# Kernel optimization log

Hardware: AMD Instinct MI355X
Metric: run time of the kernel (lower is better)

The kernel has to match this reference:

```python
import jax, jax.numpy as jnp
import numpy as np

EPS = 1e-5
N_HEAD = 16


def layernorm(x, g, b):
    mu = jnp.mean(x, axis=-1, keepdims=True)
    var = jnp.mean(jnp.square(x - mu), axis=-1, keepdims=True)
    return (x - mu) * jax.lax.rsqrt(var + EPS) * g + b


def setup_inputs() -> dict:
    key = jax.random.key(0)
    ks = jax.random.split(key, 8)
    B, S, D = 4, 2048, 1024
    F = 4 * D
    s = 0.02
    return {
        "h": jax.random.normal(ks[0], (B, S, D), jnp.float32),
        "ln1_g": jnp.ones((D,), jnp.float32),
        "ln1_b": jnp.zeros((D,), jnp.float32),
        "wq": jax.random.normal(ks[1], (D, D), jnp.float32) * s,
        "bq": jnp.zeros((D,), jnp.float32),
        "wk": jax.random.normal(ks[2], (D, D), jnp.float32) * s,
        "bk": jnp.zeros((D,), jnp.float32),
        "wv": jax.random.normal(ks[3], (D, D), jnp.float32) * s,
        "bv": jnp.zeros((D,), jnp.float32),
        "wo": jax.random.normal(ks[4], (D, D), jnp.float32) * s,
        "bo": jnp.zeros((D,), jnp.float32),
        "ln2_g": jnp.ones((D,), jnp.float32),
        "ln2_b": jnp.zeros((D,), jnp.float32),
        "wfc": jax.random.normal(ks[5], (F, D), jnp.float32) * s,
        "bfc": jnp.zeros((F,), jnp.float32),
        "wproj": jax.random.normal(ks[6], (D, F), jnp.float32) * s,
        "bproj": jnp.zeros((D,), jnp.float32),
    }


def reference(h, ln1_g, ln1_b, wq, bq, wk, bk, wv, bv, wo, bo,
              ln2_g, ln2_b, wfc, bfc, wproj, bproj):
    B, S, D = h.shape
    H = N_HEAD
    Dh = D // H

    # --- attention sub-block ---
    r = h
    x = layernorm(h, ln1_g, ln1_b)
    q = (x @ wq.T + bq).reshape(B, S, H, Dh)
    k = (x @ wk.T + bk).reshape(B, S, H, Dh)
    v = (x @ wv.T + bv).reshape(B, S, H, Dh)

    scores = jnp.einsum("bqhd,bkhd->bhqk", q, k) / jnp.sqrt(jnp.float32(Dh))
    causal = jnp.tril(jnp.ones((S, S), bool))  # [S,S]
    scores = jnp.where(causal, scores, jnp.finfo(scores.dtype).min)
    probs = jax.nn.softmax(scores, axis=-1)
    o = jnp.einsum("bhqk,bkhd->bqhd", probs, v).reshape(B, S, D)
    h = r + (o @ wo.T + bo)

    # --- MLP sub-block ---
    r = h
    x = layernorm(h, ln2_g, ln2_b)
    x = jax.nn.gelu(x @ wfc.T + bfc, approximate=True)  # NewGELU (tanh)
    h = r + (x @ wproj.T + bproj)
    return h
```

## Files before the change

kernel.cpp:

```cpp
#include <hip/hip_runtime.h>
#include <hip/hip_bf16.h>
#include <stdint.h>


typedef short bf16x8 __attribute__((ext_vector_type(8)));
typedef float f32x4  __attribute__((ext_vector_type(4)));
typedef float f32x16 __attribute__((ext_vector_type(16)));
typedef short s16x4  __attribute__((ext_vector_type(4)));

__device__ __forceinline__ short f2bf(float f) {
  union { float f; uint32_t u; } a;
  a.f = f;
  uint32_t r = a.u + 0x7fffu + ((a.u >> 16) & 1u);
  return (short)(r >> 16);
}

__device__ __forceinline__ unsigned cvt_pk_bf16(float lo, float hi_) {
  unsigned r;
  asm("v_cvt_pk_bf16_f32 %0, %1, %2" : "=v"(r) : "v"(lo), "v"(hi_));
  return r;
}

__device__ __forceinline__ float ex2(float x) {
  float r;
  asm("v_exp_f32 %0, %1" : "=v"(r) : "v"(x));
  return r;
}

__device__ __forceinline__ float rcp(float x) {
  float r;
  asm("v_rcp_f32 %0, %1" : "=v"(r) : "v"(x));
  return r;
}

__device__ __forceinline__ float m3(float a, float b, float c) {
  return fmaxf(fmaxf(a, b), c);
}

__device__ __forceinline__ void gload_lds16(const void* g, void* l) {
  __builtin_amdgcn_global_load_lds(
      (const __attribute__((address_space(1))) void*)g,
      (__attribute__((address_space(3))) void*)l, 16, 0, 0);
}

__device__ __forceinline__ float gelu_f(float x) {
  float y = 0.7978845608028654f * (x + 0.044715f * x * x * x);
  y = fminf(fmaxf(y, -20.f), 20.f);
  float e = __expf(2.f * y);
  return 0.5f * x * (1.f + (e - 1.f) / (e + 1.f));
}

struct W6 {
  const float* s[6];
  short* d[6];
  int off[7];
};

__global__ __launch_bounds__(256)
void cvt_all(W6 a) {
  const int i = blockIdx.x * 256 + threadIdx.x;
#pragma unroll
  for (int k = 0; k < 6; ++k) {
    if (i >= a.off[k] && i < a.off[k + 1]) {
      const int j = i - a.off[k];
      float4 v = ((const float4*)a.s[k])[j];
      s16x4 o;
      o[0] = f2bf(v.x); o[1] = f2bf(v.y); o[2] = f2bf(v.z); o[3] = f2bf(v.w);
      ((s16x4*)a.d[k])[j] = o;
    }
  }
}

__global__ __launch_bounds__(256)
void ln_fwd(const float* __restrict__ x, const float* __restrict__ g,
            const float* __restrict__ b, short* __restrict__ y) {
  const long row = blockIdx.x;
  const int t = threadIdx.x;
  const float4 xv = ((const float4*)(x + row * 1024))[t];
  float s  = xv.x + xv.y + xv.z + xv.w;
  float ss = xv.x * xv.x + xv.y * xv.y + xv.z * xv.z + xv.w * xv.w;
#pragma unroll
  for (int m = 1; m < 64; m <<= 1) {
    s  += __shfl_xor(s, m);
    ss += __shfl_xor(ss, m);
  }
  __shared__ float rs[4], rss[4];
  const int wid = t >> 6, lane = t & 63;
  if (lane == 0) { rs[wid] = s; rss[wid] = ss; }
  __syncthreads();
  s  = rs[0] + rs[1] + rs[2] + rs[3];
  ss = rss[0] + rss[1] + rss[2] + rss[3];
  const float mu   = s * (1.f / 1024.f);
  const float var  = ss * (1.f / 1024.f) - mu * mu;
  const float rstd = rsqrtf(var + 1e-5f);
  const float4 gv = ((const float4*)g)[t];
  const float4 bv = ((const float4*)b)[t];
  s16x4 ov;
  ov[0] = f2bf((xv.x - mu) * rstd * gv.x + bv.x);
  ov[1] = f2bf((xv.y - mu) * rstd * gv.y + bv.y);
  ov[2] = f2bf((xv.z - mu) * rstd * gv.z + bv.z);
  ov[3] = f2bf((xv.w - mu) * rstd * gv.w + bv.w);
  *(s16x4*)(y + row * 1024 + t * 4) = ov;
}

template <int OUT_BF16, int HAS_RES, int HAS_GELU, int SCALE_Q>
__global__ __launch_bounds__(256, 2)
void gemm_bt5(const short* __restrict__ A, const short* __restrict__ W,
              const float* __restrict__ bias, const float* __restrict__ res,
              void* __restrict__ out, int M, int N, int K) {
  __shared__ short As[128 * 64];
  __shared__ short Bs[256 * 64];
  const int tid = threadIdx.x;
  const int wid = tid >> 6, lane = tid & 63;
  const int l16 = lane & 15, lg = lane >> 4;
  const int wm = wid >> 1, wn = wid & 1;

  const int nbx = N >> 8;
  const int nwg = nbx * (M >> 7);
  int flat = (int)blockIdx.x;
  if ((nwg & 7) == 0) flat = (flat & 7) * (nwg >> 3) + (flat >> 3);
  const int brow = (flat / nbx) * 128, bcol = (flat % nbx) * 256;

  f32x4 acc[4][8] = {};

  const int r0 = tid >> 3, g0 = tid & 7;

  int ra[4], rb[8];
#pragma unroll
  for (int m = 0; m < 4; ++m) ra[m] = wm * 64 + m * 16 + l16;
#pragma unroll
  for (int n = 0; n < 8; ++n) rb[n] = wn * 128 + n * 16 + l16;

  for (int kt = 0; kt < K; kt += 64) {
    __syncthreads();
#pragma unroll
    for (int i = 0; i < 4; ++i) {
      const int row = i * 32 + r0;
      gload_lds16(A + (long)(brow + row) * K + kt + 8 * (g0 ^ (row & 7)),
                  &As[(i * 256 + tid) * 8]);
    }
#pragma unroll
    for (int i = 0; i < 8; ++i) {
      const int row = i * 32 + r0;
      gload_lds16(W + (long)(bcol + row) * K + kt + 8 * (g0 ^ (row & 7)),
                  &Bs[(i * 256 + tid) * 8]);
    }
    __syncthreads();

#pragma unroll
    for (int kk = 0; kk < 2; ++kk) {
      bf16x8 af[4], bf[8];
#pragma unroll
      for (int m = 0; m < 4; ++m)
        af[m] = *(const bf16x8*)&As[ra[m] * 64 + 8 * ((kk * 4 + lg) ^ (ra[m] & 7))];
#pragma unroll
      for (int n = 0; n < 8; ++n)
        bf[n] = *(const bf16x8*)&Bs[rb[n] * 64 + 8 * ((kk * 4 + lg) ^ (rb[n] & 7))];
#pragma unroll
      for (int m = 0; m < 4; ++m)
#pragma unroll
        for (int n = 0; n < 8; ++n)
          acc[m][n] = __builtin_amdgcn_mfma_f32_16x16x32_bf16(af[m], bf[n], acc[m][n], 0, 0, 0);
    }
  }

#pragma unroll
  for (int n = 0; n < 8; ++n) {
    const int col = bcol + wn * 128 + n * 16 + l16;
    const float bb = bias[col];
    const bool doScale = SCALE_Q && (col < N / 3);
#pragma unroll
    for (int m = 0; m < 4; ++m) {
#pragma unroll
      for (int j = 0; j < 4; ++j) {
        const long row = brow + wm * 64 + m * 16 + lg * 4 + j;
        float vv = acc[m][n][j] + bb;
        if (HAS_GELU) vv = gelu_f(vv);
        if (HAS_RES) vv += res[row * N + col];
        if (SCALE_Q && doScale) vv *= 0.18033688f;
        if (OUT_BF16) ((short*)out)[row * N + col] = f2bf(vv);
        else          ((float*)out)[row * N + col] = vv;
      }
    }
  }
}

template <int OUT_BF16, int HAS_RES, int HAS_GELU>
__global__ __launch_bounds__(256, 2)
void gemm_bt6(const short* __restrict__ A, const short* __restrict__ W,
              const float* __restrict__ bias, const float* __restrict__ res,
              void* __restrict__ out, int M, int N, int K) {
  __shared__ short As[128 * 64];
  __shared__ short Bs[128 * 64];
  const int tid = threadIdx.x;
  const int wid = tid >> 6, lane = tid & 63;
  const int l16 = lane & 15, lg = lane >> 4;
  const int wm = wid >> 1, wn = wid & 1;

  const int nbx = N >> 7;
  const int nwg = nbx * (M >> 7);
  int flat = (int)blockIdx.x;
  if ((nwg & 7) == 0) flat = (flat & 7) * (nwg >> 3) + (flat >> 3);
  const int brow = (flat / nbx) * 128, bcol = (flat % nbx) * 128;

  f32x4 acc[4][4] = {};

  const int r0 = tid >> 3, g0 = tid & 7;

  int ra[4], rb[4];
#pragma unroll
  for (int m = 0; m < 4; ++m) ra[m] = wm * 64 + m * 16 + l16;
#pragma unroll
  for (int n = 0; n < 4; ++n) rb[n] = wn * 64 + n * 16 + l16;

  for (int kt = 0; kt < K; kt += 64) {
    __syncthreads();
#pragma unroll
    for (int i = 0; i < 4; ++i) {
      const int row = i * 32 + r0;
      gload_lds16(A + (long)(brow + row) * K + kt + 8 * (g0 ^ (row & 7)),
                  &As[(i * 256 + tid) * 8]);
      gload_lds16(W + (long)(bcol + row) * K + kt + 8 * (g0 ^ (row & 7)),
                  &Bs[(i * 256 + tid) * 8]);
    }
    __syncthreads();

#pragma unroll
    for (int kk = 0; kk < 2; ++kk) {
      bf16x8 af[4], bf[4];
#pragma unroll
      for (int m = 0; m < 4; ++m)
        af[m] = *(const bf16x8*)&As[ra[m] * 64 + 8 * ((kk * 4 + lg) ^ (ra[m] & 7))];
#pragma unroll
      for (int n = 0; n < 4; ++n)
        bf[n] = *(const bf16x8*)&Bs[rb[n] * 64 + 8 * ((kk * 4 + lg) ^ (rb[n] & 7))];
#pragma unroll
      for (int m = 0; m < 4; ++m)
#pragma unroll
        for (int n = 0; n < 4; ++n)
          acc[m][n] = __builtin_amdgcn_mfma_f32_16x16x32_bf16(af[m], bf[n], acc[m][n], 0, 0, 0);
    }
  }

#pragma unroll
  for (int n = 0; n < 4; ++n) {
    const int col = bcol + wn * 64 + n * 16 + l16;
    const float bb = bias[col];
#pragma unroll
    for (int m = 0; m < 4; ++m) {
#pragma unroll
      for (int j = 0; j < 4; ++j) {
        const long row = brow + wm * 64 + m * 16 + lg * 4 + j;
        float vv = acc[m][n][j] + bb;
        if (HAS_GELU) vv = gelu_f(vv);
        if (HAS_RES) vv += res[row * N + col];
        if (OUT_BF16) ((short*)out)[row * N + col] = f2bf(vv);
        else          ((float*)out)[row * N + col] = vv;
      }
    }
  }
}

__global__ __launch_bounds__(256)
void transpose_v(const short* __restrict__ v, short* __restrict__ vtg,
                 int S, int ldv, int H) {
  __shared__ short t[64][66];
  const int bh = blockIdx.y, b = bh / H, hh = bh % H;
  const int s0 = blockIdx.x * 64;
  const int tid = threadIdx.x;
#pragma unroll
  for (int i = 0; i < 2; ++i) {
    const int c = i * 256 + tid;
    const int sl = c >> 3, d8 = (c & 7) * 8;
    bf16x8 vv = *(const bf16x8*)&v[((long)b * S + s0 + sl) * ldv + hh * 64 + d8];
#pragma unroll
    for (int j = 0; j < 8; ++j) t[d8 + j][sl] = vv[j];
  }
  __syncthreads();
#pragma unroll
  for (int i = 0; i < 2; ++i) {
    const int c = i * 256 + tid;
    const int dl = c >> 3, s8 = (c & 7) * 8;
    bf16x8 ov;
#pragma unroll
    for (int j = 0; j < 8; ++j) ov[j] = t[dl][s8 + j];
    *(bf16x8*)&vtg[((long)bh * 64 + dl) * S + s0 + s8] = ov;
  }
}

__global__ __launch_bounds__(256, 4)
void attn_fwd2(const short* __restrict__ qg, const short* __restrict__ kg,
               const short* __restrict__ vtg, short* __restrict__ og,
               int S, int ldq, int D, int H) {
  const int tid = threadIdx.x, wid = tid >> 6, lane = tid & 63;
  const int l31 = lane & 31, hi = lane >> 5;
  const int fid = blockIdx.x;
  const int bh = fid & 63;
  const int b = bh / H, hh = bh % H;
  static const int perm[16] = {15, 0, 8, 7, 1, 14, 6, 9, 13, 2, 10, 5, 3, 12, 4, 11};
  const int qt = perm[(fid >> 6) & 15];
  const int q0 = qt * 128;
  const long qbase = (long)b * S * ldq + hh * 64;
  const long obase = (long)b * S * D + hh * 64;
  const long vbase = (long)bh * 64 * S;

  __shared__ short Ks[2][64 * 64];
  __shared__ short Vs[2][64 * 64];

  auto STAGE = [&](int buf, int k0) {
#pragma unroll
    for (int i = 0; i < 2; ++i) {
      const int c = i * 256 + tid;
      const int row = c >> 3, gl = c & 7;
      gload_lds16(&kg[qbase + (long)(k0 + row) * ldq + 8 * (gl ^ (row & 7))],
                  &Ks[buf][(i * 256 + wid * 64) * 8]);
      gload_lds16(&vtg[vbase + (long)row * S + k0 + 8 * (gl ^ (row & 7))],
                  &Vs[buf][(i * 256 + wid * 64) * 8]);
    }
  };

  const int qw = q0 + wid * 32;
  const int qv = qw + l31;

  bf16x8 qf[4];
#pragma unroll
  for (int s = 0; s < 4; ++s)
    qf[s] = *(const bf16x8*)&qg[qbase + (long)qv * ldq + 16 * s + 8 * hi];

  f32x16 oa[2] = {};
  float mr = -3000.f, lr = 0.f;

  const int ntiles = qt * 2 + 2;

  STAGE(0, 0);
  for (int t = 0; t < ntiles; ++t) {
    const int cur = t & 1;
    const int k0 = t * 64;
    if (t + 1 < ntiles) {
      STAGE(cur ^ 1, k0 + 64);
      asm volatile("s_waitcnt vmcnt(4)" ::: "memory");
    } else {
      asm volatile("s_waitcnt vmcnt(0)" ::: "memory");
    }
    __builtin_amdgcn_s_barrier();

    if (k0 < qw + 32) {
      f32x16 st[2] = {};
#pragma unroll
      for (int s = 0; s < 4; ++s) {
        const int g = ((s << 1) | hi) ^ (l31 & 7);
        bf16x8 kf0 = *(const bf16x8*)&Ks[cur][l31 * 64 + 8 * g];
        bf16x8 kf1 = *(const bf16x8*)&Ks[cur][(32 + l31) * 64 + 8 * g];
        st[0] = __builtin_amdgcn_mfma_f32_32x32x16_bf16(kf0, qf[s], st[0], 0, 0, 0);
        st[1] = __builtin_amdgcn_mfma_f32_32x32x16_bf16(kf1, qf[s], st[1], 0, 0, 0);
      }

      const bool need_mask = (k0 + 63 > qw);
      float pv[2][16];
#pragma unroll
      for (int kb = 0; kb < 2; ++kb)
#pragma unroll
        for (int r = 0; r < 16; ++r) {
          float v = st[kb][r];
          if (need_mask) {
            const int key = k0 + kb * 32 + (r & 3) + 8 * (r >> 2) + 4 * hi;
            if (key > qv) v = -1e30f;
          }
          pv[kb][r] = v;
        }

      float rm = fmaxf(pv[0][0], pv[0][1]);
#pragma unroll
      for (int r = 2; r < 16; r += 2) rm = m3(rm, pv[0][r], pv[0][r + 1]);
#pragma unroll
      for (int r = 0; r < 16; r += 2) rm = m3(rm, pv[1][r], pv[1][r + 1]);
      rm = fmaxf(rm, __shfl_xor(rm, 32));

      const bool defer = (bool)__all(rm <= mr + 8.f);
      const float mn = defer ? mr : fmaxf(mr, rm);

      float a0 = 0.f, a1 = 0.f, a2 = 0.f, a3 = 0.f;
#pragma unroll
      for (int r = 0; r < 8; ++r) {
        float p0 = ex2(pv[0][r] - mn);      pv[0][r] = p0;      a0 += p0;
        float p1 = ex2(pv[0][8 + r] - mn);  pv[0][8 + r] = p1;  a1 += p1;
        float p2 = ex2(pv[1][r] - mn);      pv[1][r] = p2;      a2 += p2;
        float p3 = ex2(pv[1][8 + r] - mn);  pv[1][8 + r] = p3;  a3 += p3;
      }
      float ls = (a0 + a1) + (a2 + a3);
      ls += __shfl_xor(ls, 32);

      if (!defer) {
        const float alpha = ex2(mr - mn);
        lr = lr * alpha + ls;
        mr = mn;
#pragma unroll
        for (int r = 0; r < 16; ++r) {
          const int crow = (r & 3) + 8 * (r >> 2) + 4 * hi;
          const float ar = __shfl(alpha, crow | (lane & 32));
          oa[0][r] *= ar;
          oa[1][r] *= ar;
        }
      } else {
        lr += ls;
      }

      bf16x8 pa[4];
#pragma unroll
      for (int kb = 0; kb < 2; ++kb) {
        unsigned pk[8], ex[8];
#pragma unroll
        for (int i2 = 0; i2 < 8; ++i2)
          pk[i2] = cvt_pk_bf16(pv[kb][2 * i2], pv[kb][2 * i2 + 1]);
#pragma unroll
        for (int i2 = 0; i2 < 8; ++i2)
          ex[i2] = (unsigned)__shfl_xor((int)pk[i2], 32);
        union { unsigned u[4]; bf16x8 v8; } f0, f1;
        f0.u[0] = hi ? ex[2] : pk[0];
        f0.u[1] = hi ? ex[3] : pk[1];
        f0.u[2] = hi ? pk[2] : ex[0];
        f0.u[3] = hi ? pk[3] : ex[1];
        f1.u[0] = hi ? ex[6] : pk[4];
        f1.u[1] = hi ? ex[7] : pk[5];
        f1.u[2] = hi ? pk[6] : ex[4];
        f1.u[3] = hi ? pk[7] : ex[5];
        pa[2 * kb]     = f0.v8;
        pa[2 * kb + 1] = f1.v8;
      }

#pragma unroll
      for (int s = 0; s < 4; ++s) {
        const int g = ((s << 1) | hi) ^ (l31 & 7);
        bf16x8 vf0 = *(const bf16x8*)&Vs[cur][l31 * 64 + 8 * g];
        bf16x8 vf1 = *(const bf16x8*)&Vs[cur][(32 + l31) * 64 + 8 * g];
        oa[0] = __builtin_amdgcn_mfma_f32_32x32x16_bf16(pa[s], vf0, oa[0], 0, 0, 0);
        oa[1] = __builtin_amdgcn_mfma_f32_32x32x16_bf16(pa[s], vf1, oa[1], 0, 0, 0);
      }
    }

    asm volatile("s_waitcnt lgkmcnt(0)" ::: "memory");
    __builtin_amdgcn_s_barrier();
  }

  const float linv = rcp(lr);
#pragma unroll
  for (int r = 0; r < 16; ++r) {
    const int crow = (r & 3) + 8 * (r >> 2) + 4 * hi;
    const float li = __shfl(linv, crow | (lane & 32));
    const long row = qw + crow;
    og[obase + row * D + l31]      = f2bf(oa[0][r] * li);
    og[obase + row * D + 32 + l31] = f2bf(oa[1][r] * li);
  }
}

extern "C" void kernel_launch(void* const* d_in, const int* in_sizes, int n_in,
                              void* d_out, int out_size, void* d_ws, size_t ws_size,
                              hipStream_t stream) {
  (void)in_sizes; (void)n_in; (void)out_size; (void)ws_size;
  const float* h     = (const float*)d_in[0];
  const float* ln1_g = (const float*)d_in[1];
  const float* ln1_b = (const float*)d_in[2];
  const float* wq    = (const float*)d_in[3];
  const float* bq    = (const float*)d_in[4];
  const float* wk    = (const float*)d_in[5];
  const float* bk    = (const float*)d_in[6];
  const float* wv    = (const float*)d_in[7];
  const float* bv    = (const float*)d_in[8];
  const float* wo    = (const float*)d_in[9];
  const float* bo    = (const float*)d_in[10];
  const float* ln2_g = (const float*)d_in[11];
  const float* ln2_b = (const float*)d_in[12];
  const float* wfc   = (const float*)d_in[13];
  const float* bfc   = (const float*)d_in[14];
  const float* wproj = (const float*)d_in[15];
  const float* bproj = (const float*)d_in[16];

  const int B = 4, S = 2048, D = 1024, H = 16, F = 4096, T = B * S;
  const int D3 = 3 * D;

  char* ws = (char*)d_ws;
  size_t off = 0;
  auto alloc = [&](size_t bytes) {
    void* p = ws + off;
    off += (bytes + 255) & ~(size_t)255;
    return p;
  };
  short* xb   = (short*)alloc((size_t)T * D * 2);
  short* qkv  = (short*)alloc((size_t)T * D3 * 2);
  short* ob   = (short*)alloc((size_t)T * D * 2);
  float* h2   = (float*)alloc((size_t)T * D * 4);
  short* wqkvb  = (short*)alloc((size_t)D3 * D * 2);
  short* wob    = (short*)alloc((size_t)D * D * 2);
  short* wfcb   = (short*)alloc((size_t)F * D * 2);
  short* wprojb = (short*)alloc((size_t)D * F * 2);
  float* bqkv   = (float*)alloc((size_t)D3 * 4);
  short* ub  = qkv;
  short* vtg = (short*)h2;

  W6 wargs;
  const int nqq = D * D / 4;
  wargs.s[0] = wq;    wargs.d[0] = wqkvb;
  wargs.s[1] = wk;    wargs.d[1] = wqkvb + (size_t)D * D;
  wargs.s[2] = wv;    wargs.d[2] = wqkvb + (size_t)2 * D * D;
  wargs.s[3] = wo;    wargs.d[3] = wob;
  wargs.s[4] = wfc;   wargs.d[4] = wfcb;
  wargs.s[5] = wproj; wargs.d[5] = wprojb;
  wargs.off[0] = 0;
  wargs.off[1] = nqq;
  wargs.off[2] = 2 * nqq;
  wargs.off[3] = 3 * nqq;
  wargs.off[4] = 4 * nqq;
  wargs.off[5] = 4 * nqq + F * D / 4;
  wargs.off[6] = 4 * nqq + 2 * (F * D / 4);
  cvt_all<<<dim3(wargs.off[6] / 256), 256, 0, stream>>>(wargs);
  hipMemcpyAsync(bqkv,         bq, D * 4, hipMemcpyDeviceToDevice, stream);
  hipMemcpyAsync(bqkv + D,     bk, D * 4, hipMemcpyDeviceToDevice, stream);
  hipMemcpyAsync(bqkv + 2 * D, bv, D * 4, hipMemcpyDeviceToDevice, stream);

  ln_fwd<<<dim3(T), 256, 0, stream>>>(h, ln1_g, ln1_b, xb);
  gemm_bt5<1, 0, 0, 1><<<dim3((T / 128) * (D3 / 256)), 256, 0, stream>>>(
      xb, wqkvb, bqkv, nullptr, qkv, T, D3, D);
  transpose_v<<<dim3(S / 64, B * H), 256, 0, stream>>>(qkv + 2 * D, vtg, S, D3, H);
  attn_fwd2<<<dim3((S / 128) * (B * H / 64) * 64), 256, 0, stream>>>(
      qkv, qkv + D, vtg, ob, S, D3, D, H);
  gemm_bt6<0, 1, 0><<<dim3((T / 128) * (D / 128)), 256, 0, stream>>>(
      ob, wob, bo, h, h2, T, D, D);

  ln_fwd<<<dim3(T), 256, 0, stream>>>(h2, ln2_g, ln2_b, xb);
  gemm_bt5<1, 0, 1, 0><<<dim3((T / 128) * (F / 256)), 256, 0, stream>>>(
      xb, wfcb, bfc, nullptr, ub, T, F, D);
  gemm_bt6<0, 1, 0><<<dim3((T / 128) * (D / 128)), 256, 0, stream>>>(
      ub, wprojb, bproj, h2, (float*)d_out, T, D, F);
}
```

Baseline: 372.8 us.

## Replace QKV/FC GEMM with 256x256 double-buffered 8-wave pipelined kernel

Replaces the 128x256-tile, 4-wave GEMM used for the QKV and FC projections with a 256x256-tile, 512-thread kernel. It double-buffers A and B tiles in LDS and interleaves the global-to-LDS prefetch of the next K tiles with MFMA phases, using explicit barriers, waitcnts and setprio. The aim is to hide load latency and raise arithmetic intensity per tile. It uses 128KB of LDS per block, which limits occupancy, and produces fewer blocks: 384 for the QKV GEMM and 512 for FC. That risks poor wave balance across CUs.

Result: slower. 392.2 us (+5.2%).

```diff
diff --git a/kernel.cpp b/kernel.cpp
--- a/kernel.cpp
+++ b/kernel.cpp
@@ -104,82 +104,157 @@
 }
 
 template <int OUT_BF16, int HAS_RES, int HAS_GELU, int SCALE_Q>
-__global__ __launch_bounds__(256, 2)
-void gemm_bt5(const short* __restrict__ A, const short* __restrict__ W,
+__global__ __launch_bounds__(512, 2)
+void gemm256b(const short* __restrict__ A, const short* __restrict__ W,
               const float* __restrict__ bias, const float* __restrict__ res,
               void* __restrict__ out, int M, int N, int K) {
-  __shared__ short As[128 * 64];
-  __shared__ short Bs[256 * 64];
+  __shared__ short As[2][256 * 64];
+  __shared__ short Bs[2][256 * 64];
   const int tid = threadIdx.x;
   const int wid = tid >> 6, lane = tid & 63;
   const int l16 = lane & 15, lg = lane >> 4;
-  const int wm = wid >> 1, wn = wid & 1;
+  const int wm = wid >> 2, wn = wid & 3;
 
   const int nbx = N >> 8;
-  const int nwg = nbx * (M >> 7);
+  const int nwg = nbx * (M >> 8);
   int flat = (int)blockIdx.x;
   if ((nwg & 7) == 0) flat = (flat & 7) * (nwg >> 3) + (flat >> 3);
-  const int brow = (flat / nbx) * 128, bcol = (flat % nbx) * 256;
-
-  f32x4 acc[4][8] = {};
+  const int brow = (flat / nbx) * 256, bcol = (flat % nbx) * 256;
+
+  f32x4 acc[2][4][4] = {};
 
   const int r0 = tid >> 3, g0 = tid & 7;
 
-  int ra[4], rb[8];
-#pragma unroll
-  for (int m = 0; m < 4; ++m) ra[m] = wm * 64 + m * 16 + l16;
-#pragma unroll
-  for (int n = 0; n < 8; ++n) rb[n] = wn * 128 + n * 16 + l16;
-
-  for (int kt = 0; kt < K; kt += 64) {
-    __syncthreads();
-#pragma unroll
-    for (int i = 0; i < 4; ++i) {
-      const int row = i * 32 + r0;
+  auto STAGE_A = [&](int buf, int half, int kt) {
+#pragma unroll
+    for (int i = 0; i < 2; ++i) {
+      const int row = half * 128 + i * 64 + r0;
       gload_lds16(A + (long)(brow + row) * K + kt + 8 * (g0 ^ (row & 7)),
-                  &As[(i * 256 + tid) * 8]);
-    }
-#pragma unroll
-    for (int i = 0; i < 8; ++i) {
-      const int row = i * 32 + r0;
+                  &As[buf][(half * 1024 + i * 512 + tid) * 8]);
+    }
+  };
+  auto STAGE_B = [&](int buf, int half, int kt) {
+#pragma unroll
+    for (int i = 0; i < 2; ++i) {
+      const int row = half * 128 + i * 64 + r0;
       gload_lds16(W + (long)(bcol + row) * K + kt + 8 * (g0 ^ (row & 7)),
-                  &Bs[(i * 256 + tid) * 8]);
-    }
-    __syncthreads();
-
-#pragma unroll
-    for (int kk = 0; kk < 2; ++kk) {
-      bf16x8 af[4], bf[8];
-#pragma unroll
-      for (int m = 0; m < 4; ++m)
-        af[m] = *(const bf16x8*)&As[ra[m] * 64 + 8 * ((kk * 4 + lg) ^ (ra[m] & 7))];
-#pragma unroll
-      for (int n = 0; n < 8; ++n)
-        bf[n] = *(const bf16x8*)&Bs[rb[n] * 64 + 8 * ((kk * 4 + lg) ^ (rb[n] & 7))];
-#pragma unroll
-      for (int m = 0; m < 4; ++m)
-#pragma unroll
-        for (int n = 0; n < 8; ++n)
-          acc[m][n] = __builtin_amdgcn_mfma_f32_16x16x32_bf16(af[m], bf[n], acc[m][n], 0, 0, 0);
-    }
-  }
-
-#pragma unroll
-  for (int n = 0; n < 8; ++n) {
-    const int col = bcol + wn * 128 + n * 16 + l16;
+                  &Bs[buf][(half * 1024 + i * 512 + tid) * 8]);
+    }
+  };
+
+  int ra0[4], ra1[4], rb[4];
+#pragma unroll
+  for (int m = 0; m < 4; ++m) {
+    ra0[m] = wm * 128 + m * 16 + l16;
+    ra1[m] = ra0[m] + 64;
+  }
+#pragma unroll
+  for (int n = 0; n < 4; ++n) rb[n] = wn * 64 + n * 16 + l16;
+
+  const int NT = K >> 6;
+  STAGE_A(0, 0, 0); STAGE_A(0, 1, 0); STAGE_B(0, 0, 0); STAGE_B(0, 1, 0);
+  STAGE_B(1, 0, 64); STAGE_B(1, 1, 64);
+  asm volatile("s_waitcnt vmcnt(4)" ::: "memory");
+  __builtin_amdgcn_s_barrier();
+
+  for (int t = 0; t < NT; ++t) {
+    const int c = t & 1;
+    const bool s1 = (t + 1 < NT), s2 = (t + 2 < NT);
+    const int kt1 = (t + 1) << 6, kt2 = (t + 2) << 6;
+
+    bf16x8 a[4], b[4];
+
+#pragma unroll
+    for (int n = 0; n < 4; ++n)
+      b[n] = *(const bf16x8*)&Bs[c][rb[n] * 64 + 8 * (lg ^ (rb[n] & 7))];
+#pragma unroll
+    for (int m = 0; m < 4; ++m)
+      a[m] = *(const bf16x8*)&As[c][ra0[m] * 64 + 8 * (lg ^ (ra0[m] & 7))];
+    if (s1) STAGE_A(c ^ 1, 0, kt1);
+    __builtin_amdgcn_s_barrier();
+    asm volatile("s_waitcnt lgkmcnt(0)" ::: "memory");
+    __builtin_amdgcn_sched_barrier(0);
+    __builtin_amdgcn_s_setprio(1);
+#pragma unroll
+    for (int m = 0; m < 4; ++m)
+#pragma unroll
+      for (int n = 0; n < 4; ++n)
+        acc[0][m][n] = __builtin_amdgcn_mfma_f32_16x16x32_bf16(a[m], b[n], acc[0][m][n], 0, 0, 0);
+    __builtin_amdgcn_s_setprio(0);
+    __builtin_amdgcn_s_barrier();
+
+#pragma unroll
+    for (int m = 0; m < 4; ++m)
+      a[m] = *(const bf16x8*)&As[c][ra1[m] * 64 + 8 * (lg ^ (ra1[m] & 7))];
+    if (s1) STAGE_A(c ^ 1, 1, kt1);
+    __builtin_amdgcn_s_barrier();
+    asm volatile("s_waitcnt lgkmcnt(0)" ::: "memory");
+    __builtin_amdgcn_sched_barrier(0);
+    __builtin_amdgcn_s_setprio(1);
+#pragma unroll
+    for (int m = 0; m < 4; ++m)
+#pragma unroll
+      for (int n = 0; n < 4; ++n)
+        acc[1][m][n] = __builtin_amdgcn_mfma_f32_16x16x32_bf16(a[m], b[n], acc[1][m][n], 0, 0, 0);
+    __builtin_amdgcn_s_setprio(0);
+    __builtin_amdgcn_s_barrier();
+
+#pragma unroll
+    for (int n = 0; n < 4; ++n)
+      b[n] = *(const bf16x8*)&Bs[c][rb[n] * 64 + 8 * ((4 + lg) ^ (rb[n] & 7))];
+#pragma unroll
+    for (int m = 0; m < 4; ++m)
+      a[m] = *(const bf16x8*)&As[c][ra0[m] * 64 + 8 * ((4 + lg) ^ (ra0[m] & 7))];
+    __builtin_amdgcn_s_barrier();
+    asm volatile("s_waitcnt lgkmcnt(0)" ::: "memory");
+    __builtin_amdgcn_sched_barrier(0);
+    __builtin_amdgcn_s_setprio(1);
+#pragma unroll
+    for (int m = 0; m < 4; ++m)
+#pragma unroll
+      for (int n = 0; n < 4; ++n)
+        acc[0][m][n] = __builtin_amdgcn_mfma_f32_16x16x32_bf16(a[m], b[n], acc[0][m][n], 0, 0, 0);
+    __builtin_amdgcn_s_setprio(0);
+    __builtin_amdgcn_s_barrier();
+
+#pragma unroll
+    for (int m = 0; m < 4; ++m)
+      a[m] = *(const bf16x8*)&As[c][ra1[m] * 64 + 8 * ((4 + lg) ^ (ra1[m] & 7))];
+    if (s2) { STAGE_B(c, 0, kt2); STAGE_B(c, 1, kt2); }
+    __builtin_amdgcn_s_barrier();
+    asm volatile("s_waitcnt lgkmcnt(0)" ::: "memory");
+    __builtin_amdgcn_sched_barrier(0);
+    __builtin_amdgcn_s_setprio(1);
+#pragma unroll
+    for (int m = 0; m < 4; ++m)
+#pragma unroll
+      for (int n = 0; n < 4; ++n)
+        acc[1][m][n] = __builtin_amdgcn_mfma_f32_16x16x32_bf16(a[m], b[n], acc[1][m][n], 0, 0, 0);
+    __builtin_amdgcn_s_setprio(0);
+    if (s2)      asm volatile("s_waitcnt vmcnt(4)" ::: "memory");
+    else if (s1) asm volatile("s_waitcnt vmcnt(0)" ::: "memory");
+    __builtin_amdgcn_s_barrier();
+  }
+
+#pragma unroll
+  for (int n = 0; n < 4; ++n) {
+    const int col = bcol + wn * 64 + n * 16 + l16;
     const float bb = bias[col];
     const bool doScale = SCALE_Q && (col < N / 3);
 #pragma unroll
-    for (int m = 0; m < 4; ++m) {
-#pragma unroll
-      for (int j = 0; j < 4; ++j) {
-        const long row = brow + wm * 64 + m * 16 + lg * 4 + j;
-        float vv = acc[m][n][j] + bb;
-        if (HAS_GELU) vv = gelu_f(vv);
-        if (HAS_RES) vv += res[row * N + col];
-        if (SCALE_Q && doScale) vv *= 0.18033688f;
-        if (OUT_BF16) ((short*)out)[row * N + col] = f2bf(vv);
-        else          ((float*)out)[row * N + col] = vv;
+    for (int mh = 0; mh < 2; ++mh) {
+#pragma unroll
+      for (int m = 0; m < 4; ++m) {
+#pragma unroll
+        for (int j = 0; j < 4; ++j) {
+          const long row = brow + wm * 128 + mh * 64 + m * 16 + lg * 4 + j;
+          float vv = acc[mh][m][n][j] + bb;
+          if (HAS_GELU) vv = gelu_f(vv);
+          if (HAS_RES) vv += res[row * N + col];
+          if (SCALE_Q && doScale) vv *= 0.18033688f;
+          if (OUT_BF16) ((short*)out)[row * N + col] = f2bf(vv);
+          else          ((float*)out)[row * N + col] = vv;
+        }
       }
     }
   }
@@ -518,7 +593,7 @@
   hipMemcpyAsync(bqkv + 2 * D, bv, D * 4, hipMemcpyDeviceToDevice, stream);
 
   ln_fwd<<<dim3(T), 256, 0, stream>>>(h, ln1_g, ln1_b, xb);
-  gemm_bt5<1, 0, 0, 1><<<dim3((T / 128) * (D3 / 256)), 256, 0, stream>>>(
+  gemm256b<1, 0, 0, 1><<<dim3((T / 256) * (D3 / 256)), 512, 0, stream>>>(
       xb, wqkvb, bqkv, nullptr, qkv, T, D3, D);
   transpose_v<<<dim3(S / 64, B * H), 256, 0, stream>>>(qkv + 2 * D, vtg, S, D3, H);
   attn_fwd2<<<dim3((S / 128) * (B * H / 64) * 64), 256, 0, stream>>>(
@@ -527,7 +602,7 @@
       ob, wob, bo, h, h2, T, D, D);
 
   ln_fwd<<<dim3(T), 256, 0, stream>>>(h2, ln2_g, ln2_b, xb);
-  gemm_bt5<1, 0, 1, 0><<<dim3((T / 128) * (F / 256)), 256, 0, stream>>>(
+  gemm256b<1, 0, 1, 0><<<dim3((T / 256) * (F / 256)), 512, 0, stream>>>(
       xb, wfcb, bfc, nullptr, ub, T, F, D);
   gemm_bt6<0, 1, 0><<<dim3((T / 128) * (D / 128)), 256, 0, stream>>>(
       ub, wprojb, bproj, h2, (float*)d_out, T, D, F);
```
